# Optimization experiments

Measured on AMD Instinct MI355X. Metric: run time of the kernel, lower is better.

The kernel has to match this reference:

```python
import jax, jax.numpy as jnp
import numpy as np

B, N, T, D, H = 32, 64, 16, 256, 256  # batch, actors, frames, feat dim, hidden_dim


def setup_inputs() -> dict:
    key = jax.random.key(0)
    ks = jax.random.split(key, 6)
    s = lambda fan: 1.0 / np.sqrt(fan)
    return {
        "x": jax.random.normal(ks[0], (B, N, T, D), jnp.float32),
        "W1_t": jax.random.normal(ks[1], (T * D, H), jnp.float32) * s(T * D),
        "b1_t": jnp.zeros((H,), jnp.float32),
        "W2_t": jax.random.normal(ks[2], (H, H), jnp.float32) * s(H),
        "b2_t": jnp.zeros((H,), jnp.float32),
        "W1_i": jax.random.normal(ks[3], (2 * H, H), jnp.float32) * s(2 * H),
        "b1_i": jnp.zeros((H,), jnp.float32),
        "W2_i": jax.random.normal(ks[4], (H, H), jnp.float32) * s(H),
        "b2_i": jnp.zeros((H,), jnp.float32),
    }


def reference(x, W1_t, b1_t, W2_t, b2_t, W1_i, b1_i, W2_i, b2_i):
    b, n, t, d = x.shape
    # STTR_trans output is immediately detached in the original; modeled as
    # identity + stop_gradient (view(N,B,T,-1) then view-back is a no-op on data).
    pf = jax.lax.stop_gradient(x)  # [B, N, T, D]

    # time_track_projection: MLP(T*D -> H -> H), ReLU between layers, no BN, eval dropout.
    h = jax.nn.relu(pf.reshape(b * n, t * d) @ W1_t + b1_t)
    person_feature = (h @ W2_t + b2_t).reshape(b, n, -1)  # [B, N, H]

    # relation_indexes: row-major enumeration of ordered pairs (i, j), j != i.
    # tem1 row N*i+j holds feature i, tem2 row N*i+j holds feature j.
    ii, jj = np.nonzero(~np.eye(n, dtype=bool))  # each [N*(N-1)], row-major order
    pair = jnp.concatenate(
        [person_feature[:, ii, :], person_feature[:, jj, :]], axis=-1
    )  # [B, N*(N-1), 2H] -- gather avoids materializing the full N*N grid

    # interaction_track_projection: MLP(2H -> H -> H)
    hi = jax.nn.relu(pair @ W1_i + b1_i)
    relation_feature = hi @ W2_i + b2_i  # [B, N*(N-1), H]

    return relation_feature, pf, person_feature
```

## Files before the change

kernel.cpp:

```cpp
#include <hip/hip_runtime.h>
#include <stdint.h>

typedef unsigned short u16;
typedef __attribute__((ext_vector_type(4))) float f32x4;
typedef __attribute__((ext_vector_type(8))) short bf16x8;
typedef __attribute__((ext_vector_type(4))) unsigned short u16x4;

#define DEV static __device__ __forceinline__

DEV u16 f2bf(float f) {
  union { float f; uint32_t u; } v; v.f = f;
  uint32_t u = v.u;
  return (u16)((u + 0x7FFFu + ((u >> 16) & 1u)) >> 16);
}

DEV float bf2f(u16 u) {
  union { uint32_t u; float f; } v; v.u = ((uint32_t)u) << 16;
  return v.f;
}

__global__ __launch_bounds__(256) void k_prep(const float* __restrict__ W1t,
                                              const float* __restrict__ W2t,
                                              const float* __restrict__ W1i,
                                              const float* __restrict__ W2i,
                                              const float* __restrict__ b2t,
                                              const float* __restrict__ b1i,
                                              u16* __restrict__ W1T,
                                              u16* __restrict__ W2iT,
                                              u16* __restrict__ WcatT,
                                              float* __restrict__ biascat) {
  __shared__ u16 tile[64][65];
  __shared__ float col[256];
  int b = blockIdx.x;
  int t = threadIdx.x;
  if (b < 272) {
    const float* in;
    u16* out;
    int R, C, bb;
    if (b < 256) { in = W1t; out = W1T; R = 4096; C = 256; bb = b; }
    else         { in = W2i; out = W2iT; R = 256;  C = 256; bb = b - 256; }
    int tr = (bb >> 2) * 64, tc = (bb & 3) * 64;
    int lr = t & 63;
    #pragma unroll
    for (int it = 0; it < 16; ++it) {
      int r = it * 4 + (t >> 6);
      tile[r][lr] = f2bf(in[(tr + r) * C + tc + lr]);
    }
    __syncthreads();
    #pragma unroll
    for (int it = 0; it < 16; ++it) {
      int c = it * 4 + (t >> 6);
      out[(tc + c) * R + tr + lr] = tile[lr][c];
    }
    return;
  }
  if (b < 1040) {
    int n = b - 272;
    int k = t;
    if (n < 256) {
      WcatT[n * 256 + k] = f2bf(W2t[k * 256 + n]);
      return;
    }
    int off = (n < 512) ? 0 : 256;
    int c = n & 255;
    col[k] = W1i[(off + k) * 256 + c];
    __syncthreads();
    const float* wrow = W2t + k * 256;
    const float* cp = col;
    f32x4 acc4 = {};
    #pragma unroll 4
    for (int m = 0; m < 64; ++m) {
      f32x4 wv = *(const f32x4*)(wrow + m * 4);
      f32x4 cv = *(const f32x4*)(cp + m * 4);
      acc4 += wv * cv;
    }
    float acc = acc4[0] + acc4[1] + acc4[2] + acc4[3];
    WcatT[n * 256 + k] = f2bf(acc);
    return;
  }
  int n = (b - 1040) * 256 + t;
  float v;
  if (n < 256) {
    v = b2t[n];
  } else {
    int off = (n < 512) ? 0 : 256;
    int c = n & 255;
    float acc = (n < 512) ? 0.f : b1i[c];
    for (int k = 0; k < 256; ++k) acc += b2t[k] * W1i[(off + k) * 256 + c];
    v = acc;
  }
  biascat[n] = v;
}

__global__ __launch_bounds__(256, 4) void k_gemm1f(const float* __restrict__ x,
                                                   float* __restrict__ pf,
                                                   const u16* __restrict__ BT,
                                                   u16* __restrict__ part) {
  __shared__ u16 As[32][520];
  int t = threadIdx.x;
  int m0 = blockIdx.x * 32;
  int k0 = blockIdx.y * 512;
  {
    int row = t >> 3;
    int cb = (t & 7) * 4;
    const float* src = x + (m0 + row) * 4096 + k0;
    float* dst = pf + (m0 + row) * 4096 + k0;
    #pragma unroll
    for (int j = 0; j < 16; ++j) {
      f32x4 v = *(const f32x4*)(src + cb + j * 32);
      *(f32x4*)(dst + cb + j * 32) = v;
      u16x4 o;
      #pragma unroll
      for (int e = 0; e < 4; ++e) o[e] = f2bf(v[e]);
      *(u16x4*)(&As[row][cb + j * 32]) = o;
    }
  }
  __syncthreads();
  int w = t >> 6, l = t & 63;
  int n0 = w * 64;
  int koff = (l >> 4) * 8;
  const u16* pb0 = BT + (n0 + (l & 15)) * 4096 + k0 + koff;
  int ar = l & 15;
  f32x4 acc[2][4] = {};
  for (int ks = 0; ks < 16; ++ks) {
    bf16x8 a[2];
    #pragma unroll
    for (int mf = 0; mf < 2; ++mf)
      a[mf] = *(const bf16x8*)(&As[ar + mf * 16][koff + ks * 32]);
    #pragma unroll
    for (int nf = 0; nf < 4; ++nf) {
      bf16x8 b = *(const bf16x8*)(pb0 + nf * 16 * 4096 + ks * 32);
      #pragma unroll
      for (int mf = 0; mf < 2; ++mf)
        acc[mf][nf] = __builtin_amdgcn_mfma_f32_16x16x32_bf16(b, a[mf], acc[mf][nf], 0, 0, 0);
    }
  }
  u16* out = part + blockIdx.y * (2048 * 256);
  #pragma unroll
  for (int mf = 0; mf < 2; ++mf) {
    int row = m0 + mf * 16 + (l & 15);
    #pragma unroll
    for (int nf = 0; nf < 4; ++nf) {
      int colv = n0 + nf * 16 + ((l >> 4) * 4);
      u16x4 o;
      #pragma unroll
      for (int r = 0; r < 4; ++r) o[r] = f2bf(acc[mf][nf][r]);
      *(u16x4*)(out + row * 256 + colv) = o;
    }
  }
}

__global__ __launch_bounds__(256) void k_reduce_h(const u16* __restrict__ part,
                                                  const float* __restrict__ b1t,
                                                  u16* __restrict__ hb) {
  int i = blockIdx.x * 256 + threadIdx.x;
  int e = i * 4;
  f32x4 s = {};
  #pragma unroll
  for (int z = 0; z < 8; ++z) {
    u16x4 p = *(const u16x4*)(part + z * (2048 * 256) + e);
    #pragma unroll
    for (int r = 0; r < 4; ++r) s[r] += bf2f(p[r]);
  }
  f32x4 bb = *(const f32x4*)(b1t + (e & 255));
  u16x4 o;
  #pragma unroll
  for (int r = 0; r < 4; ++r) o[r] = f2bf(fmaxf(s[r] + bb[r], 0.f));
  *(u16x4*)(hb + e) = o;
}

__global__ __launch_bounds__(256, 4) void k_gemm3(const u16* __restrict__ A,
                                                  const u16* __restrict__ BT,
                                                  const float* __restrict__ biascat,
                                                  float* __restrict__ person,
                                                  u16* __restrict__ Apr,
                                                  u16* __restrict__ Bpr) {
  int w = threadIdx.x >> 6, l = threadIdx.x & 63;
  int row = blockIdx.x * 64 + w * 16 + (l & 15);
  int coln = blockIdx.y * 64;
  int k0 = (l >> 4) * 8;
  const u16* pa = A + row * 256 + k0;
  const u16* pb0 = BT + (coln + (l & 15)) * 256 + k0;
  f32x4 acc[4] = {};
  #pragma unroll
  for (int ks = 0; ks < 8; ++ks) {
    bf16x8 a = *(const bf16x8*)(pa + ks * 32);
    #pragma unroll
    for (int nf = 0; nf < 4; ++nf) {
      bf16x8 b = *(const bf16x8*)(pb0 + nf * 16 * 256 + ks * 32);
      acc[nf] = __builtin_amdgcn_mfma_f32_16x16x32_bf16(b, a, acc[nf], 0, 0, 0);
    }
  }
  if (coln < 256) {
    #pragma unroll
    for (int nf = 0; nf < 4; ++nf) {
      int lc = nf * 16 + ((l >> 4) * 4);
      f32x4 bias4 = *(const f32x4*)(biascat + coln + lc);
      *(f32x4*)(person + row * 256 + coln + lc) = acc[nf] + bias4;
    }
  } else {
    u16* dst = (coln < 512) ? Apr : Bpr;
    int cbase = (coln < 512) ? coln - 256 : coln - 512;
    #pragma unroll
    for (int nf = 0; nf < 4; ++nf) {
      int lc = nf * 16 + ((l >> 4) * 4);
      f32x4 bias4 = *(const f32x4*)(biascat + coln + lc);
      f32x4 v = acc[nf] + bias4;
      u16x4 o;
      #pragma unroll
      for (int r = 0; r < 4; ++r) o[r] = f2bf(v[r]);
      *(u16x4*)(dst + row * 256 + cbase + lc) = o;
    }
  }
}

__global__ __launch_bounds__(512, 4) void k_pair_gemm(const u16* __restrict__ Apr,
                                                      const u16* __restrict__ Bpr,
                                                      const u16* __restrict__ W2iT,
                                                      const float* __restrict__ b2i,
                                                      float* __restrict__ rel) {
  __shared__ u16 hi[128 * 264];
  int t = threadIdx.x;
  int lane = t & 63;
  int R0 = blockIdx.x * 128;
  {
    int r = t >> 6;
    int R = R0 + r;
    int b = R / 4032;
    int q = R - b * 4032;
    int i = q / 63;
    int rem = q - i * 63;
    #pragma unroll
    for (int it = 0; it < 16; ++it) {
      int j = rem + (rem >= i ? 1 : 0);
      u16x4 ua = *(const u16x4*)(Apr + (b * 64 + i) * 256 + lane * 4);
      u16x4 ub = *(const u16x4*)(Bpr + (b * 64 + j) * 256 + lane * 4);
      u16x4 o;
      #pragma unroll
      for (int e = 0; e < 4; ++e) o[e] = f2bf(fmaxf(bf2f(ua[e]) + bf2f(ub[e]), 0.f));
      *(u16x4*)(&hi[r * 264 + lane * 4]) = o;
      r += 8;
      rem += 8;
      if (rem >= 63) {
        rem -= 63;
        ++i;
        if (i >= 64) { i = 0; ++b; }
      }
    }
  }
  __syncthreads();
  int wid = t >> 6;
  int wr = wid >> 2, wc = wid & 3;
  f32x4 acc[4][4] = {};
  int arow0 = wr * 64 + (lane & 15);
  int koff = (lane >> 4) * 8;
  const u16* pb0 = W2iT + (wc * 64 + (lane & 15)) * 256 + koff;
  for (int ks = 0; ks < 8; ++ks) {
    bf16x8 a[4];
    #pragma unroll
    for (int mf = 0; mf < 4; ++mf)
      a[mf] = *(const bf16x8*)(&hi[(arow0 + mf * 16) * 264 + ks * 32 + koff]);
    #pragma unroll
    for (int nf = 0; nf < 4; ++nf) {
      bf16x8 b = *(const bf16x8*)(pb0 + nf * 16 * 256 + ks * 32);
      #pragma unroll
      for (int mf = 0; mf < 4; ++mf)
        acc[mf][nf] = __builtin_amdgcn_mfma_f32_16x16x32_bf16(b, a[mf], acc[mf][nf], 0, 0, 0);
    }
  }
  f32x4 bias4[4];
  #pragma unroll
  for (int nf = 0; nf < 4; ++nf)
    bias4[nf] = *(const f32x4*)(b2i + wc * 64 + nf * 16 + ((lane >> 4) * 4));
  #pragma unroll
  for (int mf = 0; mf < 4; ++mf) {
    int row = R0 + wr * 64 + mf * 16 + (lane & 15);
    #pragma unroll
    for (int nf = 0; nf < 4; ++nf) {
      int gc = wc * 64 + nf * 16 + ((lane >> 4) * 4);
      *(f32x4*)(rel + row * 256 + gc) = acc[mf][nf] + bias4[nf];
    }
  }
}


extern "C" void kernel_launch(void* const* d_in, const int* in_sizes, int n_in,
                              void* d_out, int out_size, void* d_ws, size_t ws_size,
                              hipStream_t stream) {
  const float* x   = (const float*)d_in[0];
  const float* W1t = (const float*)d_in[1];
  const float* b1t = (const float*)d_in[2];
  const float* W2t = (const float*)d_in[3];
  const float* b2t = (const float*)d_in[4];
  const float* W1i = (const float*)d_in[5];
  const float* b1i = (const float*)d_in[6];
  const float* W2i = (const float*)d_in[7];
  const float* b2i = (const float*)d_in[8];

  float* out = (float*)d_out;
  float* rel = out;
  float* pf = out + 33030144;
  float* person = out + 41418752;

  char* ws = (char*)d_ws;
  u16*   W1T     = (u16*)(ws + 0);
  u16*   WcatT   = (u16*)(ws + 2097152);
  u16*   W2iT    = (u16*)(ws + 2490368);
  float* biascat = (float*)(ws + 2621440);
  u16*   h_bf    = (u16*)(ws + 2625536);
  u16*   Apr     = (u16*)(ws + 3674112);
  u16*   Bpr     = (u16*)(ws + 4722688);
  u16*   part    = (u16*)(ws + 5771264);

  k_prep<<<1043, 256, 0, stream>>>(W1t, W2t, W1i, W2i, b2t, b1i,
                                   W1T, W2iT, WcatT, biascat);
  k_gemm1f<<<dim3(64, 8), 256, 0, stream>>>(x, pf, W1T, part);
  k_reduce_h<<<512, 256, 0, stream>>>(part, b1t, h_bf);
  k_gemm3<<<dim3(32, 12), 256, 0, stream>>>(h_bf, WcatT, biascat, person, Apr, Bpr);
  k_pair_gemm<<<1008, 512, 0, stream>>>(Apr, Bpr, W2iT, b2i, rel);
}
```

Measured before the change: 121.7 us.

## Build pair-MLP A fragments directly from global loads, dropping LDS staging

The pair GEMM kernel no longer stages the relu(A_i + B_j) hidden tile in shared memory behind a barrier. Each lane now computes its own MFMA A-fragment straight from global Apr/Bpr rows, using precomputed per-row offsets. It packs the values with the hardware v_cvt_pk_bf16_f32 instruction instead of software rounding. This removes the LDS footprint, the barrier and the LDS traffic, which may raise occupancy. In exchange, the 4 column-warps of a block each recompute the same A rows and issue redundant small global loads.

New measurement: 151.9 us. +24.8%, slower.

```diff
diff --git a/kernel.cpp b/kernel.cpp
--- a/kernel.cpp
+++ b/kernel.cpp
@@ -219,47 +219,46 @@
                                                       const u16* __restrict__ W2iT,
                                                       const float* __restrict__ b2i,
                                                       float* __restrict__ rel) {
-  __shared__ u16 hi[128 * 264];
   int t = threadIdx.x;
   int lane = t & 63;
   int R0 = blockIdx.x * 128;
-  {
-    int r = t >> 6;
-    int R = R0 + r;
+  int wid = t >> 6;
+  int wr = wid >> 2, wc = wid & 3;
+  int koff = (lane >> 4) * 8;
+  int offA[4], offB[4];
+  #pragma unroll
+  for (int mf = 0; mf < 4; ++mf) {
+    int R = R0 + wr * 64 + mf * 16 + (lane & 15);
     int b = R / 4032;
     int q = R - b * 4032;
     int i = q / 63;
     int rem = q - i * 63;
-    #pragma unroll
-    for (int it = 0; it < 16; ++it) {
-      int j = rem + (rem >= i ? 1 : 0);
-      u16x4 ua = *(const u16x4*)(Apr + (b * 64 + i) * 256 + lane * 4);
-      u16x4 ub = *(const u16x4*)(Bpr + (b * 64 + j) * 256 + lane * 4);
-      u16x4 o;
-      #pragma unroll
-      for (int e = 0; e < 4; ++e) o[e] = f2bf(fmaxf(bf2f(ua[e]) + bf2f(ub[e]), 0.f));
-      *(u16x4*)(&hi[r * 264 + lane * 4]) = o;
-      r += 8;
-      rem += 8;
-      if (rem >= 63) {
-        rem -= 63;
-        ++i;
-        if (i >= 64) { i = 0; ++b; }
-      }
-    }
-  }
-  __syncthreads();
-  int wid = t >> 6;
-  int wr = wid >> 2, wc = wid & 3;
+    int j = rem + (rem >= i ? 1 : 0);
+    offA[mf] = (b * 64 + i) * 256 + koff;
+    offB[mf] = (b * 64 + j) * 256 + koff;
+  }
   f32x4 acc[4][4] = {};
-  int arow0 = wr * 64 + (lane & 15);
-  int koff = (lane >> 4) * 8;
   const u16* pb0 = W2iT + (wc * 64 + (lane & 15)) * 256 + koff;
   for (int ks = 0; ks < 8; ++ks) {
     bf16x8 a[4];
     #pragma unroll
-    for (int mf = 0; mf < 4; ++mf)
-      a[mf] = *(const bf16x8*)(&hi[(arow0 + mf * 16) * 264 + ks * 32 + koff]);
+    for (int mf = 0; mf < 4; ++mf) {
+      u16x4 ua0 = *(const u16x4*)(Apr + offA[mf] + ks * 32);
+      u16x4 ua1 = *(const u16x4*)(Apr + offA[mf] + ks * 32 + 4);
+      u16x4 ub0 = *(const u16x4*)(Bpr + offB[mf] + ks * 32);
+      u16x4 ub1 = *(const u16x4*)(Bpr + offB[mf] + ks * 32 + 4);
+      float s[8];
+      #pragma unroll
+      for (int e = 0; e < 4; ++e) {
+        s[e]     = fmaxf(bf2f(ua0[e]) + bf2f(ub0[e]), 0.f);
+        s[e + 4] = fmaxf(bf2f(ua1[e]) + bf2f(ub1[e]), 0.f);
+      }
+      union { bf16x8 v; uint32_t w[4]; } pk;
+      #pragma unroll
+      for (int p = 0; p < 4; ++p)
+        asm("v_cvt_pk_bf16_f32 %0, %1, %2" : "=v"(pk.w[p]) : "v"(s[2 * p]), "v"(s[2 * p + 1]));
+      a[mf] = pk.v;
+    }
     #pragma unroll
     for (int nf = 0; nf < 4; ++nf) {
       bf16x8 b = *(const bf16x8*)(pb0 + nf * 16 * 256 + ks * 32);
```
